# Optimization experiments

Measured on AMD Instinct MI355X. Metric: run time of the kernel, lower is better.

The kernel has to match this reference:

```python
import jax, jax.numpy as jnp
import numpy as np

D_MODEL, N_HEADS, D_VALUE = 512, 8, 64
D_HEAD = D_MODEL // N_HEADS


def setup_inputs() -> dict:
    key = jax.random.key(0)
    ks = jax.random.split(key, 5)
    B, T = 2, 2048
    x = jax.random.normal(ks[0], (B, T, D_MODEL), dtype=jnp.float32)
    # torch nn.Linear convention: W has shape [out_features, in_features]
    scale = 0.02
    W_q = jax.random.normal(ks[1], (N_HEADS * D_HEAD, D_MODEL), dtype=jnp.float32) * scale
    W_k = jax.random.normal(ks[2], (N_HEADS * D_HEAD, D_MODEL), dtype=jnp.float32) * scale
    W_v = jax.random.normal(ks[3], (N_HEADS * D_VALUE, D_MODEL), dtype=jnp.float32) * scale
    W_out = jax.random.normal(ks[4], (D_MODEL, N_HEADS * D_VALUE), dtype=jnp.float32) * scale
    return {"x": x, "W_q": W_q, "W_k": W_k, "W_v": W_v, "W_out": W_out}


def _elu_feature_map(t):
    # phi(t) = elu(t) + 1
    return jax.nn.elu(t) + 1.0


def reference(x, W_q, W_k, W_v, W_out):
    B, T, D = x.shape
    H, dh, dv = N_HEADS, D_HEAD, D_VALUE
    # projections (Linear without bias: x @ W.T)
    Q = _elu_feature_map((x @ W_q.T).reshape(B, T, H, dh)).transpose(0, 2, 1, 3)  # [B,H,T,dh]
    K = _elu_feature_map((x @ W_k.T).reshape(B, T, H, dh)).transpose(0, 2, 1, 3)  # [B,H,T,dh]
    V = (x @ W_v.T).reshape(B, T, H, dv).transpose(0, 2, 1, 3)                    # [B,H,T,dv]
    # causal linear attention via cumulative outer-product state
    KV = jnp.einsum('bhti,bhtj->bhtij', K, V)       # [B,H,T,dh,dv]
    S = jnp.cumsum(KV, axis=2)                      # running state
    z = jnp.cumsum(K, axis=2)                       # running normalizer
    num = jnp.einsum('bhti,bhtij->bhtj', Q, S)      # [B,H,T,dv]
    den = jnp.maximum(jnp.einsum('bhti,bhti->bht', Q, z), 1e-6)[..., None]
    out = (num / den).transpose(0, 2, 1, 3).reshape(B, T, H * dv)
    return out @ W_out.T
```

## Files before the change

### kernel.cpp

```cpp
#include <hip/hip_runtime.h>
#include <hip/hip_bf16.h>

#define T_SEQ 2048
#define BATCH 2
#define DMODEL 512
#define NHEAD 8
#define DHEAD 64
#define DVAL 64
#define BH 16
#define CHUNK 64
#define NCHUNK 32
#define MROWS 4096

typedef __bf16 bf16;
typedef __bf16 bf16x8 __attribute__((ext_vector_type(8)));
typedef __bf16 bf16x4 __attribute__((ext_vector_type(4)));
typedef float f32x4 __attribute__((ext_vector_type(4)));

__device__ inline void gload_lds16(const bf16* g, bf16* l) {
  __builtin_amdgcn_global_load_lds((const __attribute__((address_space(1))) void*)g,
                                   (__attribute__((address_space(3))) void*)l, 16, 0, 0);
}

__device__ inline int sw_t(int row, int g) {
  return ((g ^ (row & 7) ^ (row >> 3)) << 3);
}

__global__ __launch_bounds__(256) void k_convert(const float* __restrict__ x,
                          const float* __restrict__ wq,
                          const float* __restrict__ wk,
                          const float* __restrict__ wv,
                          const float* __restrict__ wo,
                          bf16* __restrict__ x_bf,
                          bf16* __restrict__ wqkv_bf,
                          bf16* __restrict__ wo_bf) {
  const int W = DMODEL * DMODEL;
  int i = blockIdx.x * 256 + threadIdx.x;
  {
    f32x4 v = ((const f32x4*)x)[i];
    bf16x4 o; o[0] = (bf16)v[0]; o[1] = (bf16)v[1]; o[2] = (bf16)v[2]; o[3] = (bf16)v[3];
    *(bf16x4*)(x_bf + (size_t)i * 4) = o;
  }
  if (i < W / 4) {
    f32x4 a = ((const f32x4*)wq)[i];
    f32x4 b = ((const f32x4*)wk)[i];
    f32x4 c = ((const f32x4*)wv)[i];
    f32x4 d = ((const f32x4*)wo)[i];
    bf16x4 oa, ob, oc, od;
#pragma unroll
    for (int u = 0; u < 4; u++) { oa[u] = (bf16)a[u]; ob[u] = (bf16)b[u]; oc[u] = (bf16)c[u]; od[u] = (bf16)d[u]; }
    *(bf16x4*)(wqkv_bf + (size_t)i * 4) = oa;
    *(bf16x4*)(wqkv_bf + W + (size_t)i * 4) = ob;
    *(bf16x4*)(wqkv_bf + 2 * W + (size_t)i * 4) = oc;
    *(bf16x4*)(wo_bf + (size_t)i * 4) = od;
  }
}

template <int EPI>
__global__ __launch_bounds__(256) void k_gemm(const bf16* __restrict__ A,
                                              const bf16* __restrict__ B,
                                              bf16* __restrict__ Q,
                                              bf16* __restrict__ K,
                                              bf16* __restrict__ V,
                                              float* __restrict__ out) {
  __shared__ bf16 sh[12288];
  bf16* As = sh;
  bf16* Bs = sh + 4096;
  const int tid = threadIdx.x;
  const int wvi = tid >> 6, lane = tid & 63;
  const int c = lane & 15, quad = lane >> 4;
  const int m_tile = blockIdx.x * 64, n_tile = blockIdx.y * 128;
  const int r8 = lane >> 3, gp = lane & 7;
  const bf16* Abase = A + (size_t)m_tile * DMODEL;
  const bf16* Bbase = B + (size_t)n_tile * DMODEL;
  const int wn = wvi * 32;

  f32x4 acc[4][2] = {};

  for (int k0 = 0; k0 < DMODEL; k0 += 64) {
    if (k0) __syncthreads();
#pragma unroll
    for (int r = 0; r < 2; r++) {
      int t8 = wvi * 2 + r;
      const bf16* ga = Abase + (size_t)(t8 * 8 + r8) * DMODEL + k0 + ((gp ^ r8) << 3);
      gload_lds16(ga, As + t8 * 8 * 64);
    }
#pragma unroll
    for (int r = 0; r < 4; r++) {
      int t8 = wvi * 4 + r;
      const bf16* gb = Bbase + (size_t)(t8 * 8 + r8) * DMODEL + k0 + ((gp ^ r8) << 3);
      gload_lds16(gb, Bs + t8 * 8 * 64);
    }
    __syncthreads();
#pragma unroll
    for (int ks = 0; ks < 2; ks++) {
      bf16x8 af[4], bfr[2];
#pragma unroll
      for (int i = 0; i < 4; i++)
        af[i] = *(const bf16x8*)(As + (i * 16 + c) * 64 + (((ks * 4 + quad) ^ (c & 7)) << 3));
#pragma unroll
      for (int j = 0; j < 2; j++)
        bfr[j] = *(const bf16x8*)(Bs + (wn + j * 16 + c) * 64 + (((ks * 4 + quad) ^ (c & 7)) << 3));
#pragma unroll
      for (int i = 0; i < 4; i++)
#pragma unroll
        for (int j = 0; j < 2; j++)
          acc[i][j] = __builtin_amdgcn_mfma_f32_16x16x32_bf16(af[i], bfr[j], acc[i][j], 0, 0, 0);
    }
  }

  if (EPI == 0) {
    const bool is_qk = (n_tile < 1024);
    __syncthreads();
#pragma unroll
    for (int i = 0; i < 4; i++)
#pragma unroll
      for (int j = 0; j < 2; j++)
#pragma unroll
        for (int r = 0; r < 4; r++) {
          int row = i * 16 + quad * 4 + r;
          int col = wn + j * 16 + c;
          float v = acc[i][j][r];
          if (is_qk) v = (v > 0.f) ? (v + 1.f) : __expf(v);
          sh[row * 132 + col] = (bf16)v;
        }
    __syncthreads();
    bf16* dst = (n_tile < 512) ? Q : ((n_tile < 1024) ? K : V);
    int nb = n_tile & 511;
#pragma unroll
    for (int q = 0; q < 4; q++) {
      int row = q * 16 + (tid >> 4);
      int col0 = (tid & 15) * 8;
      bf16x8 v8 = *(const bf16x8*)(sh + row * 132 + col0);
      *(bf16x8*)(dst + (size_t)(m_tile + row) * 512 + nb + col0) = v8;
    }
  } else {
    float* shf = (float*)sh;
#pragma unroll
    for (int p = 0; p < 2; p++) {
      __syncthreads();
#pragma unroll
      for (int i2 = 0; i2 < 2; i2++) {
        int i = 2 * p + i2;
#pragma unroll
        for (int j = 0; j < 2; j++)
#pragma unroll
          for (int r = 0; r < 4; r++)
            shf[(i2 * 16 + quad * 4 + r) * 132 + wn + j * 16 + c] = acc[i][j][r];
      }
      __syncthreads();
      int row = tid >> 3, col0 = (tid & 7) * 16;
#pragma unroll
      for (int q4 = 0; q4 < 4; q4++) {
        f32x4 v4 = *(const f32x4*)(shf + row * 132 + col0 + q4 * 4);
        *(f32x4*)(out + (size_t)(m_tile + p * 32 + row) * 512 + n_tile + col0 + q4 * 4) = v4;
      }
    }
  }
}

__global__ __launch_bounds__(256) void k_state(const bf16* __restrict__ K,
                                               const bf16* __restrict__ V,
                                               bf16* __restrict__ KVs,
                                               float* __restrict__ zsum) {
  __shared__ bf16 Kt[4096];
  __shared__ bf16 Vt[4096];
  int chunk = blockIdx.x, bh = blockIdx.y;
  int b = bh >> 3, h = bh & 7;
  int tid = threadIdx.x, lane = tid & 63, wvi = tid >> 6;
  int rowbase = b * T_SEQ + chunk * CHUNK;

#pragma unroll
  for (int p = 0; p < 2; p++) {
    int r = p * 32 + (tid >> 3);
    int j0 = (tid & 7) * 8;
    bf16x8 kk  = *(const bf16x8*)(K + (size_t)(rowbase + r) * 512 + h * 64 + j0);
    bf16x8 vvv = *(const bf16x8*)(V + (size_t)(rowbase + r) * 512 + h * 64 + j0);
#pragma unroll
    for (int u = 0; u < 8; u++) {
      int row = j0 + u;
      Kt[row * 64 + sw_t(row, r >> 3) + (r & 7)] = kk[u];
      Vt[row * 64 + sw_t(row, r >> 3) + (r & 7)] = vvv[u];
    }
  }
  __syncthreads();

  int c = lane & 15, quad = lane >> 4;
  f32x4 acc[4] = {};
#pragma unroll
  for (int ks = 0; ks < 2; ks++) {
    int ar = wvi * 16 + c;
    bf16x8 a = *(const bf16x8*)(Vt + ar * 64 + sw_t(ar, ks * 4 + quad));
#pragma unroll
    for (int f = 0; f < 4; f++) {
      int br = f * 16 + c;
      bf16x8 bb = *(const bf16x8*)(Kt + br * 64 + sw_t(br, ks * 4 + quad));
      acc[f] = __builtin_amdgcn_mfma_f32_16x16x32_bf16(a, bb, acc[f], 0, 0, 0);
    }
  }
  bf16* op = KVs + ((size_t)(bh * NCHUNK + chunk) << 12);
  bf16x8 lo, hi;
#pragma unroll
  for (int u = 0; u < 8; u++) {
    lo[u] = (bf16)acc[u >> 2][u & 3];
    hi[u] = (bf16)acc[2 + (u >> 2)][u & 3];
  }
  *(bf16x8*)(op + tid * 16) = lo;
  *(bf16x8*)(op + tid * 16 + 8) = hi;

  if (tid < 64) {
    float s = 0.f;
#pragma unroll
    for (int g = 0; g < 8; g++) {
      bf16x8 kr = *(const bf16x8*)(Kt + tid * 64 + sw_t(tid, g));
#pragma unroll
      for (int u = 0; u < 8; u++) s += (float)kr[u];
    }
    zsum[(size_t)(bh * NCHUNK + chunk) * 64 + tid] = s;
  }
}

__global__ __launch_bounds__(256) void k_attn(const bf16* __restrict__ Q,
                                              const bf16* __restrict__ K,
                                              const bf16* __restrict__ V,
                                              const bf16* __restrict__ KVs,
                                              const float* __restrict__ zsum,
                                              bf16* __restrict__ O) {
  __shared__ bf16 SH[20480];
  bf16* Qs   = SH;
  bf16* Ks   = SH + 4096;
  bf16* Vt   = SH + 8192;
  bf16* Asm  = SH + 12288;
  bf16* Spre = SH + 16384;
  __shared__ float zp4[4][64];
  __shared__ float zpre[64], rsum[64], den[64];

  int chunk = blockIdx.x, bh = blockIdx.y;
  int b = bh >> 3, h = bh & 7;
  int tid = threadIdx.x, lane = tid & 63, wvi = tid >> 6;
  int c = lane & 15, quad = lane >> 4;
  int rowbase = b * T_SEQ + chunk * CHUNK;

#pragma unroll
  for (int p = 0; p < 2; p++) {
    int rbase = p * 32 + wvi * 8;
    int r8 = lane >> 3, gp = lane & 7;
    const bf16* gq = Q + (size_t)(rowbase + rbase + r8) * 512 + h * 64 + ((gp ^ r8) << 3);
    const bf16* gk = K + (size_t)(rowbase + rbase + r8) * 512 + h * 64 + ((gp ^ r8) << 3);
    gload_lds16(gq, Qs + rbase * 64);
    gload_lds16(gk, Ks + rbase * 64);
  }

#pragma unroll
  for (int p = 0; p < 2; p++) {
    int r = p * 32 + (tid >> 3);
    int j0 = (tid & 7) * 8;
    bf16x8 vvv = *(const bf16x8*)(V + (size_t)(rowbase + r) * 512 + h * 64 + j0);
#pragma unroll
    for (int u = 0; u < 8; u++) {
      int row = j0 + u;
      Vt[row * 64 + sw_t(row, r >> 3) + (r & 7)] = vvv[u];
    }
  }

  {
    float accp[16];
#pragma unroll
    for (int u = 0; u < 16; u++) accp[u] = 0.f;
    const bf16* base = KVs + ((size_t)(bh * NCHUNK) << 12) + tid * 16;
    for (int cc = 0; cc < chunk; cc++) {
      const bf16* pp = base + ((size_t)cc << 12);
      bf16x8 a0 = *(const bf16x8*)pp;
      bf16x8 a1 = *(const bf16x8*)(pp + 8);
#pragma unroll
      for (int u = 0; u < 8; u++) { accp[u] += (float)a0[u]; accp[8 + u] += (float)a1[u]; }
    }
#pragma unroll
    for (int s = 0; s < 16; s++) {
      int rowp = wvi * 16 + quad * 4 + (s & 3);
      int colp = (s >> 2) * 16 + c;
      Spre[rowp * 64 + sw_t(rowp, colp >> 3) + (colp & 7)] = (bf16)accp[s];
    }
  }
  {
    int i = tid & 63, qq = tid >> 6;
    float s = 0.f;
    for (int cc = qq; cc < chunk; cc += 4)
      s += zsum[(size_t)(bh * NCHUNK + cc) * 64 + i];
    zp4[qq][i] = s;
  }
  __syncthreads();
  if (tid < 64) zpre[tid] = zp4[0][tid] + zp4[1][tid] + zp4[2][tid] + zp4[3][tid];

  f32x4 sacc[4] = {};
#pragma unroll
  for (int ks = 0; ks < 2; ks++) {
    int ar = 16 * wvi + c;
    bf16x8 a = *(const bf16x8*)(Qs + ar * 64 + (((ks * 4 + quad) ^ (c & 7)) << 3));
#pragma unroll
    for (int j = 0; j < 4; j++) {
      int br = 16 * j + c;
      bf16x8 bb = *(const bf16x8*)(Ks + br * 64 + (((ks * 4 + quad) ^ (c & 7)) << 3));
      sacc[j] = __builtin_amdgcn_mfma_f32_16x16x32_bf16(a, bb, sacc[j], 0, 0, 0);
    }
  }

  float rs[4] = {0.f, 0.f, 0.f, 0.f};
#pragma unroll
  for (int j = 0; j < 4; j++) {
#pragma unroll
    for (int r = 0; r < 4; r++) {
      int t = 16 * wvi + quad * 4 + r, s = 16 * j + c;
      float v = (s <= t) ? sacc[j][r] : 0.f;
      rs[r] += v;
      Asm[t * 64 + sw_t(t, s >> 3) + (s & 7)] = (bf16)v;
    }
  }
#pragma unroll
  for (int r = 0; r < 4; r++) {
    float v = rs[r];
    v += __shfl_xor(v, 1); v += __shfl_xor(v, 2);
    v += __shfl_xor(v, 4); v += __shfl_xor(v, 8);
    if (c == 0) rsum[16 * wvi + quad * 4 + r] = v;
  }
  __syncthreads();

  if (tid < 64) {
    float s = rsum[tid];
    int t7 = tid & 7;
#pragma unroll
    for (int kg = 0; kg < 8; kg++) {
      bf16x8 qv = *(const bf16x8*)(Qs + tid * 64 + ((kg ^ t7) << 3));
#pragma unroll
      for (int u = 0; u < 8; u++) s += (float)qv[u] * zpre[kg * 8 + u];
    }
    den[tid] = fmaxf(s, 1e-6f);
  }

  f32x4 oacc[4] = {};
#pragma unroll
  for (int ks = 0; ks < 2; ks++) {
    int ar = 16 * wvi + c;
    bf16x8 aq = *(const bf16x8*)(Qs + ar * 64 + (((ks * 4 + quad) ^ (c & 7)) << 3));
    bf16x8 aa = *(const bf16x8*)(Asm + ar * 64 + sw_t(ar, ks * 4 + quad));
#pragma unroll
    for (int j = 0; j < 4; j++) {
      int br = 16 * j + c;
      bf16x8 bs = *(const bf16x8*)(Spre + br * 64 + sw_t(br, ks * 4 + quad));
      bf16x8 bv = *(const bf16x8*)(Vt + br * 64 + sw_t(br, ks * 4 + quad));
      oacc[j] = __builtin_amdgcn_mfma_f32_16x16x32_bf16(aq, bs, oacc[j], 0, 0, 0);
      oacc[j] = __builtin_amdgcn_mfma_f32_16x16x32_bf16(aa, bv, oacc[j], 0, 0, 0);
    }
  }
  __syncthreads();

  {
    bf16* shr = SH;
#pragma unroll
    for (int r = 0; r < 4; r++) {
      int t = 16 * wvi + quad * 4 + r;
      float rd = 1.f / den[t];
#pragma unroll
      for (int j = 0; j < 4; j++)
        shr[t * 76 + 16 * j + c] = (bf16)(oacc[j][r] * rd);
    }
    __syncthreads();
    int row = tid >> 2, col0 = (tid & 3) * 16;
    bf16x8 v0 = *(const bf16x8*)(shr + row * 76 + col0);
    bf16x8 v1 = *(const bf16x8*)(shr + row * 76 + col0 + 8);
    bf16* od = O + (size_t)(rowbase + row) * 512 + h * 64 + col0;
    *(bf16x8*)od = v0;
    *(bf16x8*)(od + 8) = v1;
  }
}

extern "C" void kernel_launch(void* const* d_in, const int* in_sizes, int n_in,
                              void* d_out, int out_size, void* d_ws, size_t ws_size,
                              hipStream_t stream) {
  const float* x  = (const float*)d_in[0];
  const float* wq = (const float*)d_in[1];
  const float* wk = (const float*)d_in[2];
  const float* wv = (const float*)d_in[3];
  const float* wo = (const float*)d_in[4];
  float* out = (float*)d_out;

  char* p = (char*)d_ws;
  bf16* x_bf   = (bf16*)p; p += (size_t)MROWS * DMODEL * 2;
  bf16* wqkv_b = (bf16*)p; p += (size_t)3 * DMODEL * DMODEL * 2;
  bf16* wo_b   = (bf16*)p; p += (size_t)DMODEL * DMODEL * 2;
  bf16* Qb     = (bf16*)p; p += (size_t)MROWS * 512 * 2;
  bf16* Kb     = (bf16*)p; p += (size_t)MROWS * 512 * 2;
  bf16* Vb     = (bf16*)p; p += (size_t)MROWS * 512 * 2;
  bf16* Ob     = (bf16*)p; p += (size_t)MROWS * 512 * 2;
  bf16* KVs    = (bf16*)p; p += (size_t)BH * NCHUNK * DHEAD * DVAL * 2;
  float* zs    = (float*)p; p += (size_t)BH * NCHUNK * DHEAD * 4;

  k_convert<<<2048, 256, 0, stream>>>(x, wq, wk, wv, wo, x_bf, wqkv_b, wo_b);
  k_gemm<0><<<dim3(MROWS / 64, (3 * DMODEL) / 128), 256, 0, stream>>>(
      x_bf, wqkv_b, Qb, Kb, Vb, nullptr);
  k_state<<<dim3(NCHUNK, BH), 256, 0, stream>>>(Kb, Vb, KVs, zs);
  k_attn<<<dim3(NCHUNK, BH), 256, 0, stream>>>(Qb, Kb, Vb, KVs, zs, Ob);
  k_gemm<1><<<dim3(MROWS / 64, DMODEL / 128), 256, 0, stream>>>(
      Ob, wo_b, nullptr, nullptr, nullptr, out);
}
```

Before: 113.4 us.

## Process two chunks per attention block and shrink output GEMM M-tile

The attention kernel now handles two consecutive chunks per block, carrying the prefix KV state and normalizer across them. The second chunk adds only one chunk's state instead of re-summing all earlier chunks, which cuts redundant prefix loads. The output projection GEMM is split into its own kernel with a 32-row M tile, doubling its grid to 512 blocks for better CU occupancy. The trade-off is that the attention grid is halved to 256 blocks, so each block does more serial work.

```diff
diff --git a/kernel.cpp b/kernel.cpp
--- a/kernel.cpp
+++ b/kernel.cpp
@@ -56,13 +56,11 @@
   }
 }
 
-template <int EPI>
-__global__ __launch_bounds__(256) void k_gemm(const bf16* __restrict__ A,
-                                              const bf16* __restrict__ B,
-                                              bf16* __restrict__ Q,
-                                              bf16* __restrict__ K,
-                                              bf16* __restrict__ V,
-                                              float* __restrict__ out) {
+__global__ __launch_bounds__(256) void k_gemm_qkv(const bf16* __restrict__ A,
+                                                  const bf16* __restrict__ B,
+                                                  bf16* __restrict__ Q,
+                                                  bf16* __restrict__ K,
+                                                  bf16* __restrict__ V) {
   __shared__ bf16 sh[12288];
   bf16* As = sh;
   bf16* Bs = sh + 4096;
@@ -109,53 +107,95 @@
     }
   }
 
-  if (EPI == 0) {
-    const bool is_qk = (n_tile < 1024);
+  const bool is_qk = (n_tile < 1024);
+  __syncthreads();
+#pragma unroll
+  for (int i = 0; i < 4; i++)
+#pragma unroll
+    for (int j = 0; j < 2; j++)
+#pragma unroll
+      for (int r = 0; r < 4; r++) {
+        int row = i * 16 + quad * 4 + r;
+        int col = wn + j * 16 + c;
+        float v = acc[i][j][r];
+        if (is_qk) v = (v > 0.f) ? (v + 1.f) : __expf(v);
+        sh[row * 132 + col] = (bf16)v;
+      }
+  __syncthreads();
+  bf16* dst = (n_tile < 512) ? Q : ((n_tile < 1024) ? K : V);
+  int nb = n_tile & 511;
+#pragma unroll
+  for (int q = 0; q < 4; q++) {
+    int row = q * 16 + (tid >> 4);
+    int col0 = (tid & 15) * 8;
+    bf16x8 v8 = *(const bf16x8*)(sh + row * 132 + col0);
+    *(bf16x8*)(dst + (size_t)(m_tile + row) * 512 + nb + col0) = v8;
+  }
+}
+
+__global__ __launch_bounds__(256) void k_gemm_out(const bf16* __restrict__ A,
+                                                  const bf16* __restrict__ B,
+                                                  float* __restrict__ out) {
+  __shared__ bf16 sh[10240];
+  bf16* As = sh;
+  bf16* Bs = sh + 2048;
+  const int tid = threadIdx.x;
+  const int wvi = tid >> 6, lane = tid & 63;
+  const int c = lane & 15, quad = lane >> 4;
+  const int m_tile = blockIdx.x * 32, n_tile = blockIdx.y * 128;
+  const int r8 = lane >> 3, gp = lane & 7;
+  const bf16* Abase = A + (size_t)m_tile * DMODEL;
+  const bf16* Bbase = B + (size_t)n_tile * DMODEL;
+  const int wn = wvi * 32;
+
+  f32x4 acc[2][2] = {};
+
+  for (int k0 = 0; k0 < DMODEL; k0 += 64) {
+    if (k0) __syncthreads();
+    {
+      int t8 = wvi;
+      const bf16* ga = Abase + (size_t)(t8 * 8 + r8) * DMODEL + k0 + ((gp ^ r8) << 3);
+      gload_lds16(ga, As + t8 * 8 * 64);
+    }
+#pragma unroll
+    for (int r = 0; r < 4; r++) {
+      int t8 = wvi * 4 + r;
+      const bf16* gb = Bbase + (size_t)(t8 * 8 + r8) * DMODEL + k0 + ((gp ^ r8) << 3);
+      gload_lds16(gb, Bs + t8 * 8 * 64);
+    }
     __syncthreads();
 #pragma unroll
-    for (int i = 0; i < 4; i++)
+    for (int ks = 0; ks < 2; ks++) {
+      bf16x8 af[2], bfr[2];
+#pragma unroll
+      for (int i = 0; i < 2; i++)
+        af[i] = *(const bf16x8*)(As + (i * 16 + c) * 64 + (((ks * 4 + quad) ^ (c & 7)) << 3));
 #pragma unroll
       for (int j = 0; j < 2; j++)
-#pragma unroll
-        for (int r = 0; r < 4; r++) {
-          int row = i * 16 + quad * 4 + r;
-          int col = wn + j * 16 + c;
-          float v = acc[i][j][r];
-          if (is_qk) v = (v > 0.f) ? (v + 1.f) : __expf(v);
-          sh[row * 132 + col] = (bf16)v;
-        }
-    __syncthreads();
-    bf16* dst = (n_tile < 512) ? Q : ((n_tile < 1024) ? K : V);
-    int nb = n_tile & 511;
-#pragma unroll
-    for (int q = 0; q < 4; q++) {
-      int row = q * 16 + (tid >> 4);
-      int col0 = (tid & 15) * 8;
-      bf16x8 v8 = *(const bf16x8*)(sh + row * 132 + col0);
-      *(bf16x8*)(dst + (size_t)(m_tile + row) * 512 + nb + col0) = v8;
-    }
-  } else {
-    float* shf = (float*)sh;
-#pragma unroll
-    for (int p = 0; p < 2; p++) {
-      __syncthreads();
-#pragma unroll
-      for (int i2 = 0; i2 < 2; i2++) {
-        int i = 2 * p + i2;
+        bfr[j] = *(const bf16x8*)(Bs + (wn + j * 16 + c) * 64 + (((ks * 4 + quad) ^ (c & 7)) << 3));
+#pragma unroll
+      for (int i = 0; i < 2; i++)
 #pragma unroll
         for (int j = 0; j < 2; j++)
-#pragma unroll
-          for (int r = 0; r < 4; r++)
-            shf[(i2 * 16 + quad * 4 + r) * 132 + wn + j * 16 + c] = acc[i][j][r];
-      }
-      __syncthreads();
-      int row = tid >> 3, col0 = (tid & 7) * 16;
-#pragma unroll
-      for (int q4 = 0; q4 < 4; q4++) {
-        f32x4 v4 = *(const f32x4*)(shf + row * 132 + col0 + q4 * 4);
-        *(f32x4*)(out + (size_t)(m_tile + p * 32 + row) * 512 + n_tile + col0 + q4 * 4) = v4;
-      }
-    }
+          acc[i][j] = __builtin_amdgcn_mfma_f32_16x16x32_bf16(af[i], bfr[j], acc[i][j], 0, 0, 0);
+    }
+  }
+
+  float* shf = (float*)sh;
+  __syncthreads();
+#pragma unroll
+  for (int i = 0; i < 2; i++)
+#pragma unroll
+    for (int j = 0; j < 2; j++)
+#pragma unroll
+      for (int r = 0; r < 4; r++)
+        shf[(i * 16 + quad * 4 + r) * 132 + wn + j * 16 + c] = acc[i][j][r];
+  __syncthreads();
+  int row = tid >> 3, col0 = (tid & 7) * 16;
+#pragma unroll
+  for (int q4 = 0; q4 < 4; q4++) {
+    f32x4 v4 = *(const f32x4*)(shf + row * 132 + col0 + q4 * 4);
+    *(f32x4*)(out + (size_t)(m_tile + row) * 512 + n_tile + col0 + q4 * 4) = v4;
   }
 }
 
@@ -235,45 +275,65 @@
   __shared__ float zp4[4][64];
   __shared__ float zpre[64], rsum[64], den[64];
 
-  int chunk = blockIdx.x, bh = blockIdx.y;
+  int cp = blockIdx.x, bh = blockIdx.y;
   int b = bh >> 3, h = bh & 7;
   int tid = threadIdx.x, lane = tid & 63, wvi = tid >> 6;
   int c = lane & 15, quad = lane >> 4;
-  int rowbase = b * T_SEQ + chunk * CHUNK;
-
-#pragma unroll
-  for (int p = 0; p < 2; p++) {
-    int rbase = p * 32 + wvi * 8;
-    int r8 = lane >> 3, gp = lane & 7;
-    const bf16* gq = Q + (size_t)(rowbase + rbase + r8) * 512 + h * 64 + ((gp ^ r8) << 3);
-    const bf16* gk = K + (size_t)(rowbase + rbase + r8) * 512 + h * 64 + ((gp ^ r8) << 3);
-    gload_lds16(gq, Qs + rbase * 64);
-    gload_lds16(gk, Ks + rbase * 64);
-  }
-
-#pragma unroll
-  for (int p = 0; p < 2; p++) {
-    int r = p * 32 + (tid >> 3);
-    int j0 = (tid & 7) * 8;
-    bf16x8 vvv = *(const bf16x8*)(V + (size_t)(rowbase + r) * 512 + h * 64 + j0);
-#pragma unroll
-    for (int u = 0; u < 8; u++) {
-      int row = j0 + u;
-      Vt[row * 64 + sw_t(row, r >> 3) + (r & 7)] = vvv[u];
-    }
-  }
-
-  {
-    float accp[16];
-#pragma unroll
-    for (int u = 0; u < 16; u++) accp[u] = 0.f;
-    const bf16* base = KVs + ((size_t)(bh * NCHUNK) << 12) + tid * 16;
-    for (int cc = 0; cc < chunk; cc++) {
-      const bf16* pp = base + ((size_t)cc << 12);
+  const int r8 = lane >> 3, gp = lane & 7;
+
+  float accp[16];
+#pragma unroll
+  for (int u = 0; u < 16; u++) accp[u] = 0.f;
+
+  for (int ch = 0; ch < 2; ch++) {
+    int chunk = cp * 2 + ch;
+    int rowbase = b * T_SEQ + chunk * CHUNK;
+
+    if (ch == 1) __syncthreads();
+
+#pragma unroll
+    for (int p = 0; p < 2; p++) {
+      int rbase = p * 32 + wvi * 8;
+      const bf16* gq = Q + (size_t)(rowbase + rbase + r8) * 512 + h * 64 + ((gp ^ r8) << 3);
+      const bf16* gk = K + (size_t)(rowbase + rbase + r8) * 512 + h * 64 + ((gp ^ r8) << 3);
+      gload_lds16(gq, Qs + rbase * 64);
+      gload_lds16(gk, Ks + rbase * 64);
+    }
+#pragma unroll
+    for (int p = 0; p < 2; p++) {
+      int r = p * 32 + (tid >> 3);
+      int j0 = (tid & 7) * 8;
+      bf16x8 vvv = *(const bf16x8*)(V + (size_t)(rowbase + r) * 512 + h * 64 + j0);
+#pragma unroll
+      for (int u = 0; u < 8; u++) {
+        int row = j0 + u;
+        Vt[row * 64 + sw_t(row, r >> 3) + (r & 7)] = vvv[u];
+      }
+    }
+
+    if (ch == 0) {
+      const bf16* base = KVs + ((size_t)(bh * NCHUNK) << 12) + tid * 16;
+      for (int cc = 0; cc < chunk; cc++) {
+        const bf16* pp = base + ((size_t)cc << 12);
+        bf16x8 a0 = *(const bf16x8*)pp;
+        bf16x8 a1 = *(const bf16x8*)(pp + 8);
+#pragma unroll
+        for (int u = 0; u < 8; u++) { accp[u] += (float)a0[u]; accp[8 + u] += (float)a1[u]; }
+      }
+      {
+        int i = tid & 63, qq = tid >> 6;
+        float s = 0.f;
+        for (int cc = qq; cc < chunk; cc += 4)
+          s += zsum[(size_t)(bh * NCHUNK + cc) * 64 + i];
+        zp4[qq][i] = s;
+      }
+    } else {
+      const bf16* pp = KVs + ((size_t)(bh * NCHUNK + chunk - 1) << 12) + tid * 16;
       bf16x8 a0 = *(const bf16x8*)pp;
       bf16x8 a1 = *(const bf16x8*)(pp + 8);
 #pragma unroll
       for (int u = 0; u < 8; u++) { accp[u] += (float)a0[u]; accp[8 + u] += (float)a1[u]; }
+      if (tid < 64) zpre[tid] += zsum[(size_t)(bh * NCHUNK + chunk - 1) * 64 + tid];
     }
 #pragma unroll
     for (int s = 0; s < 16; s++) {
@@ -281,96 +341,89 @@
       int colp = (s >> 2) * 16 + c;
       Spre[rowp * 64 + sw_t(rowp, colp >> 3) + (colp & 7)] = (bf16)accp[s];
     }
-  }
-  {
-    int i = tid & 63, qq = tid >> 6;
-    float s = 0.f;
-    for (int cc = qq; cc < chunk; cc += 4)
-      s += zsum[(size_t)(bh * NCHUNK + cc) * 64 + i];
-    zp4[qq][i] = s;
-  }
-  __syncthreads();
-  if (tid < 64) zpre[tid] = zp4[0][tid] + zp4[1][tid] + zp4[2][tid] + zp4[3][tid];
-
-  f32x4 sacc[4] = {};
-#pragma unroll
-  for (int ks = 0; ks < 2; ks++) {
-    int ar = 16 * wvi + c;
-    bf16x8 a = *(const bf16x8*)(Qs + ar * 64 + (((ks * 4 + quad) ^ (c & 7)) << 3));
+    __syncthreads();
+    if (ch == 0 && tid < 64) zpre[tid] = zp4[0][tid] + zp4[1][tid] + zp4[2][tid] + zp4[3][tid];
+
+    f32x4 sacc[4] = {};
+#pragma unroll
+    for (int ks = 0; ks < 2; ks++) {
+      int ar = 16 * wvi + c;
+      bf16x8 a = *(const bf16x8*)(Qs + ar * 64 + (((ks * 4 + quad) ^ (c & 7)) << 3));
+#pragma unroll
+      for (int j = 0; j < 4; j++) {
+        int br = 16 * j + c;
+        bf16x8 bb = *(const bf16x8*)(Ks + br * 64 + (((ks * 4 + quad) ^ (c & 7)) << 3));
+        sacc[j] = __builtin_amdgcn_mfma_f32_16x16x32_bf16(a, bb, sacc[j], 0, 0, 0);
+      }
+    }
+
+    float rs[4] = {0.f, 0.f, 0.f, 0.f};
 #pragma unroll
     for (int j = 0; j < 4; j++) {
-      int br = 16 * j + c;
-      bf16x8 bb = *(const bf16x8*)(Ks + br * 64 + (((ks * 4 + quad) ^ (c & 7)) << 3));
-      sacc[j] = __builtin_amdgcn_mfma_f32_16x16x32_bf16(a, bb, sacc[j], 0, 0, 0);
-    }
-  }
-
-  float rs[4] = {0.f, 0.f, 0.f, 0.f};
-#pragma unroll
-  for (int j = 0; j < 4; j++) {
+#pragma unroll
+      for (int r = 0; r < 4; r++) {
+        int t = 16 * wvi + quad * 4 + r, s = 16 * j + c;
+        float v = (s <= t) ? sacc[j][r] : 0.f;
+        rs[r] += v;
+        Asm[t * 64 + sw_t(t, s >> 3) + (s & 7)] = (bf16)v;
+      }
+    }
 #pragma unroll
     for (int r = 0; r < 4; r++) {
-      int t = 16 * wvi + quad * 4 + r, s = 16 * j + c;
-      float v = (s <= t) ? sacc[j][r] : 0.f;
-      rs[r] += v;
-      Asm[t * 64 + sw_t(t, s >> 3) + (s & 7)] = (bf16)v;
-    }
-  }
-#pragma unroll
-  for (int r = 0; r < 4; r++) {
-    float v = rs[r];
-    v += __shfl_xor(v, 1); v += __shfl_xor(v, 2);
-    v += __shfl_xor(v, 4); v += __shfl_xor(v, 8);
-    if (c == 0) rsum[16 * wvi + quad * 4 + r] = v;
-  }
-  __syncthreads();
-
-  if (tid < 64) {
-    float s = rsum[tid];
-    int t7 = tid & 7;
-#pragma unroll
-    for (int kg = 0; kg < 8; kg++) {
-      bf16x8 qv = *(const bf16x8*)(Qs + tid * 64 + ((kg ^ t7) << 3));
-#pragma unroll
-      for (int u = 0; u < 8; u++) s += (float)qv[u] * zpre[kg * 8 + u];
-    }
-    den[tid] = fmaxf(s, 1e-6f);
-  }
-
-  f32x4 oacc[4] = {};
-#pragma unroll
-  for (int ks = 0; ks < 2; ks++) {
-    int ar = 16 * wvi + c;
-    bf16x8 aq = *(const bf16x8*)(Qs + ar * 64 + (((ks * 4 + quad) ^ (c & 7)) << 3));
-    bf16x8 aa = *(const bf16x8*)(Asm + ar * 64 + sw_t(ar, ks * 4 + quad));
-#pragma unroll
-    for (int j = 0; j < 4; j++) {
-      int br = 16 * j + c;
-      bf16x8 bs = *(const bf16x8*)(Spre + br * 64 + sw_t(br, ks * 4 + quad));
-      bf16x8 bv = *(const bf16x8*)(Vt + br * 64 + sw_t(br, ks * 4 + quad));
-      oacc[j] = __builtin_amdgcn_mfma_f32_16x16x32_bf16(aq, bs, oacc[j], 0, 0, 0);
-      oacc[j] = __builtin_amdgcn_mfma_f32_16x16x32_bf16(aa, bv, oacc[j], 0, 0, 0);
-    }
-  }
-  __syncthreads();
-
-  {
-    bf16* shr = SH;
-#pragma unroll
-    for (int r = 0; r < 4; r++) {
-      int t = 16 * wvi + quad * 4 + r;
-      float rd = 1.f / den[t];
-#pragma unroll
-      for (int j = 0; j < 4; j++)
-        shr[t * 76 + 16 * j + c] = (bf16)(oacc[j][r] * rd);
+      float v = rs[r];
+      v += __shfl_xor(v, 1); v += __shfl_xor(v, 2);
+      v += __shfl_xor(v, 4); v += __shfl_xor(v, 8);
+      if (c == 0) rsum[16 * wvi + quad * 4 + r] = v;
     }
     __syncthreads();
-    int row = tid >> 2, col0 = (tid & 3) * 16;
-    bf16x8 v0 = *(const bf16x8*)(shr + row * 76 + col0);
-    bf16x8 v1 = *(const bf16x8*)(shr + row * 76 + col0 + 8);
-    bf16* od = O + (size_t)(rowbase + row) * 512 + h * 64 + col0;
-    *(bf16x8*)od = v0;
-    *(bf16x8*)(od + 8) = v1;
+
+    if (tid < 64) {
+      float s = rsum[tid];
+      int t7 = tid & 7;
+#pragma unroll
+      for (int kg = 0; kg < 8; kg++) {
+        bf16x8 qv = *(const bf16x8*)(Qs + tid * 64 + ((kg ^ t7) << 3));
+#pragma unroll
+        for (int u = 0; u < 8; u++) s += (float)qv[u] * zpre[kg * 8 + u];
+      }
+      den[tid] = fmaxf(s, 1e-6f);
+    }
+
+    f32x4 oacc[4] = {};
+#pragma unroll
+    for (int ks = 0; ks < 2; ks++) {
+      int ar = 16 * wvi + c;
+      bf16x8 aq = *(const bf16x8*)(Qs + ar * 64 + (((ks * 4 + quad) ^ (c & 7)) << 3));
+      bf16x8 aa = *(const bf16x8*)(Asm + ar * 64 + sw_t(ar, ks * 4 + quad));
+#pragma unroll
+      for (int j = 0; j < 4; j++) {
+        int br = 16 * j + c;
+        bf16x8 bs = *(const bf16x8*)(Spre + br * 64 + sw_t(br, ks * 4 + quad));
+        bf16x8 bv = *(const bf16x8*)(Vt + br * 64 + sw_t(br, ks * 4 + quad));
+        oacc[j] = __builtin_amdgcn_mfma_f32_16x16x32_bf16(aq, bs, oacc[j], 0, 0, 0);
+        oacc[j] = __builtin_amdgcn_mfma_f32_16x16x32_bf16(aa, bv, oacc[j], 0, 0, 0);
+      }
+    }
+    __syncthreads();
+
+    {
+      bf16* shr = SH;
+#pragma unroll
+      for (int r = 0; r < 4; r++) {
+        int t = 16 * wvi + quad * 4 + r;
+        float rd = 1.f / den[t];
+#pragma unroll
+        for (int j = 0; j < 4; j++)
+          shr[t * 76 + 16 * j + c] = (bf16)(oacc[j][r] * rd);
+      }
+      __syncthreads();
+      int row = tid >> 2, col0 = (tid & 3) * 16;
+      bf16x8 v0 = *(const bf16x8*)(shr + row * 76 + col0);
+      bf16x8 v1 = *(const bf16x8*)(shr + row * 76 + col0 + 8);
+      bf16* od = O + (size_t)(rowbase + row) * 512 + h * 64 + col0;
+      *(bf16x8*)od = v0;
+      *(bf16x8*)(od + 8) = v1;
+    }
   }
 }
 
@@ -396,10 +449,9 @@
   float* zs    = (float*)p; p += (size_t)BH * NCHUNK * DHEAD * 4;
 
   k_convert<<<2048, 256, 0, stream>>>(x, wq, wk, wv, wo, x_bf, wqkv_b, wo_b);
-  k_gemm<0><<<dim3(MROWS / 64, (3 * DMODEL) / 128), 256, 0, stream>>>(
-      x_bf, wqkv_b, Qb, Kb, Vb, nullptr);
+  k_gemm_qkv<<<dim3(MROWS / 64, (3 * DMODEL) / 128), 256, 0, stream>>>(
+      x_bf, wqkv_b, Qb, Kb, Vb);
   k_state<<<dim3(NCHUNK, BH), 256, 0, stream>>>(Kb, Vb, KVs, zs);
-  k_attn<<<dim3(NCHUNK, BH), 256, 0, stream>>>(Qb, Kb, Vb, KVs, zs, Ob);
-  k_gemm<1><<<dim3(MROWS / 64, DMODEL / 128), 256, 0, stream>>>(
-      Ob, wo_b, nullptr, nullptr, nullptr, out);
-}
+  k_attn<<<dim3(NCHUNK / 2, BH), 256, 0, stream>>>(Qb, Kb, Vb, KVs, zs, Ob);
+  k_gemm_out<<<dim3(MROWS / 32, DMODEL / 128), 256, 0, stream>>>(Ob, wo_b, out);
+}
```

After: 115.1 us. No clear change (+1.6%).
